# Kernel optimization log

Measured on AMD Instinct MI355X. Metric: run time of the kernel, lower is better.

Reference implementation:

```python
import jax, jax.numpy as jnp
import numpy as np

EMB = 1024
HEAD = 64
B = 4
S = 4096


def setup_inputs() -> dict:
    key = jax.random.key(0)
    ks = jax.random.split(key, 7)
    std = 1.0 / np.sqrt(EMB)
    return {
        "x": jax.random.normal(ks[0], (B, S, EMB), dtype=jnp.float32),
        "Wq": jax.random.uniform(ks[1], (EMB, HEAD), jnp.float32, -std, std),
        "bq": jax.random.uniform(ks[2], (HEAD,), jnp.float32, -std, std),
        "Wk": jax.random.uniform(ks[3], (EMB, HEAD), jnp.float32, -std, std),
        "bk": jax.random.uniform(ks[4], (HEAD,), jnp.float32, -std, std),
        "Wv": jax.random.uniform(ks[5], (EMB, HEAD), jnp.float32, -std, std),
        "bv": jax.random.uniform(ks[6], (HEAD,), jnp.float32, -std, std),
    }


def reference(x, Wq, bq, Wk, bk, Wv, bv):
    # Q, K, V: [B, S, HEAD]
    Q = x @ Wq + bq
    K = x @ Wk + bk
    V = x @ Wv + bv
    scale = 1.0 / jnp.sqrt(jnp.asarray(HEAD, dtype=Q.dtype))
    # scores: [B, S, S]
    scores = jnp.einsum("bqd,bkd->bqk", Q, K) * scale
    seq = x.shape[1]
    # original mask = tril(randn) sliced; masked_fill where mask==0 => causal
    causal = jnp.tril(jnp.ones((seq, seq), dtype=bool))
    scores = jnp.where(causal, scores, -jnp.inf)
    attn = jax.nn.softmax(scores, axis=-1)
    return jnp.einsum("bqk,bkd->bqd", attn, V)
```

## Files before the change

### kernel.cpp

```cpp
#include <hip/hip_runtime.h>
#include <stdint.h>

#define S_LEN 4096
#define EMB   1024
#define HEAD  64

typedef short bf16x8 __attribute__((ext_vector_type(8)));
typedef float f32x4  __attribute__((ext_vector_type(4)));
typedef float f32x16 __attribute__((ext_vector_type(16)));
typedef unsigned short ushort8 __attribute__((ext_vector_type(8)));

#define QSCALE 0.18033688011112042f

__device__ __forceinline__ unsigned short f2bf(float f) {
    union { float f; uint32_t u; } v; v.f = f;
    uint32_t r = v.u + 0x7fffu + ((v.u >> 16) & 1u);
    return (unsigned short)(r >> 16);
}

__device__ __forceinline__ int cvtpk_bf16(float lo, float hi_) {
    int r;
    asm("v_cvt_pk_bf16_f32 %0, %1, %2" : "=v"(r) : "v"(lo), "v"(hi_));
    return r;
}

__device__ __forceinline__ void gload_lds16(const void* g, void* l) {
    __builtin_amdgcn_global_load_lds(
        (const __attribute__((address_space(1))) void*)g,
        (__attribute__((address_space(3))) void*)l, 16, 0, 0);
}


__global__ void wprep_kernel(const float* __restrict__ Wq,
                             const float* __restrict__ Wk,
                             const float* __restrict__ Wv,
                             unsigned short* __restrict__ wt) {
    __shared__ float t[64][65];
    const int tid = threadIdx.x;
    const int m   = blockIdx.x >> 4;
    const int kcb = blockIdx.x & 15;
    const int k0  = kcb << 6;
    const float* W = (m == 0) ? Wq : (m == 1) ? Wk : Wv;
    for (int i = 0; i < 4; ++i) {
        const int k  = (tid >> 4) + i * 16;
        const int n4 = (tid & 15) << 2;
        float4 v = *(const float4*)&W[(k0 + k) * 64 + n4];
        t[k][n4 + 0] = v.x; t[k][n4 + 1] = v.y;
        t[k][n4 + 2] = v.z; t[k][n4 + 3] = v.w;
    }
    __syncthreads();
    const int n = tid >> 2, kq = (tid & 3) << 4;
    __align__(16) unsigned short u[16];
    for (int i = 0; i < 16; ++i) u[i] = f2bf(t[kq + i][n]);
    const int nimg = m * 64 + n;
    const int base = kcb * 12288 + nimg * 64;
    const int c0   = (kq >> 3) ^ (n & 7);
    const int c1   = ((kq >> 3) + 1) ^ (n & 7);
    *(int4*)&wt[base + c0 * 8] = *(int4*)&u[0];
    *(int4*)&wt[base + c1 * 8] = *(int4*)&u[8];
}

__global__ __launch_bounds__(512, 2) void qkv_kernel(
    const float* __restrict__ x, const unsigned short* __restrict__ wt,
    const float* __restrict__ bq, const float* __restrict__ bk,
    const float* __restrict__ bv,
    unsigned short* __restrict__ Qp, unsigned short* __restrict__ Kp,
    unsigned short* __restrict__ Vt) {

    __shared__ __align__(16) unsigned short xs[2][64 * 72];
    __shared__ __align__(16) unsigned short ws[2][12288];

    const int tid  = threadIdx.x;
    const int lane = tid & 63;
    const int w    = tid >> 6;
    const int wm   = w & 1;
    const int wn   = w >> 1;
    const int quad = lane >> 4;
    const int lid  = lane & 15;
    const int row0 = blockIdx.x * 64;

    f32x4 acc[2][3];
    for (int mf = 0; mf < 2; ++mf)
        for (int nf = 0; nf < 3; ++nf) acc[mf][nf] = (f32x4){0.f, 0.f, 0.f, 0.f};

#define STAGE(BUF, KC)                                                         \
    do {                                                                       \
        {             \
            int rr = tid >> 3, c8 = (tid & 7) << 3;                            \
            const float* xp = &x[(row0 + rr) * EMB + (KC) * 64 + c8];          \
            float4 v0 = *(const float4*)xp;                                    \
            float4 v1 = *(const float4*)(xp + 4);                              \
            ushort8 u;                                                         \
            u[0] = f2bf(v0.x); u[1] = f2bf(v0.y);                              \
            u[2] = f2bf(v0.z); u[3] = f2bf(v0.w);                              \
            u[4] = f2bf(v1.x); u[5] = f2bf(v1.y);                              \
            u[6] = f2bf(v1.z); u[7] = f2bf(v1.w);                              \
            *(ushort8*)&xs[BUF][rr * 72 + c8] = u;                             \
        }                                                                      \
        {          \
            const unsigned short* gs = &wt[(KC) * 12288 + w * 1536 + lane * 8];\
            gload_lds16(gs,        &ws[BUF][w * 1536]);                        \
            gload_lds16(gs +  512, &ws[BUF][w * 1536 +  512]);                 \
            gload_lds16(gs + 1024, &ws[BUF][w * 1536 + 1024]);                 \
        }                                                                      \
    } while (0)

    STAGE(0, 0);
    __syncthreads();

    for (int kc = 0; kc < 16; ++kc) {
        const int cur = kc & 1;
        if (kc + 1 < 16) STAGE(cur ^ 1, kc + 1);
        for (int kk = 0; kk < 2; ++kk) {
            bf16x8 a0 = *(const bf16x8*)&xs[cur][(wm * 32 + lid) * 72 + kk * 32 + quad * 8];
            bf16x8 a1 = *(const bf16x8*)&xs[cur][(wm * 32 + 16 + lid) * 72 + kk * 32 + quad * 8];
            const int swz = ((((kk << 2) | quad) ^ (lid & 7)) << 3);
            for (int nf = 0; nf < 3; ++nf) {
                const int n = wn * 48 + nf * 16 + lid;
                bf16x8 bfr = *(const bf16x8*)&ws[cur][n * 64 + swz];
                acc[0][nf] = __builtin_amdgcn_mfma_f32_16x16x32_bf16(a0, bfr, acc[0][nf], 0, 0, 0);
                acc[1][nf] = __builtin_amdgcn_mfma_f32_16x16x32_bf16(a1, bfr, acc[1][nf], 0, 0, 0);
            }
        }
        __syncthreads();
    }
#undef STAGE

    for (int mf = 0; mf < 2; ++mf)
        for (int nf = 0; nf < 3; ++nf) {
            const int col = wn * 48 + nf * 16 + lid;
            const int mid = col >> 6;
            const int lc  = col & 63;
            const float bias = (mid == 0) ? bq[lc] : (mid == 1) ? bk[lc] : bv[lc];
            const int rb = row0 + wm * 32 + mf * 16 + quad * 4;
            f32x4 v = acc[mf][nf];
            if (mid < 2) {
                const int base = ((rb >> 5) << 11) + ((lc >> 3) << 8)
                               + ((rb & 31) << 3) + (lc & 7);
                unsigned short* P = (mid == 0) ? Qp : Kp;
                const float sc = (mid == 0) ? QSCALE : 1.0f;
                for (int j = 0; j < 4; ++j)
                    P[base + j * 8] = f2bf((v[j] + bias) * sc);
            } else {
                const int bb = rb >> 12, s = rb & 4095;
                ushort4 u;
                u.x = f2bf(v[0] + bias); u.y = f2bf(v[1] + bias);
                u.z = f2bf(v[2] + bias); u.w = f2bf(v[3] + bias);
                *(ushort4*)&Vt[bb * 262144 + (s >> 3) * 512 + lc * 8 + (s & 7)] = u;
            }
        }
}

__global__ __launch_bounds__(1024, 1) void flash_kernel(
    const unsigned short* __restrict__ Qp, const unsigned short* __restrict__ Kp,
    const unsigned short* __restrict__ Vt, float* __restrict__ out) {

    __shared__ __align__(16) float Obuf[16][32][66];
    __shared__ float lbuf[16][32];

    const int tid  = threadIdx.x;
    const int lane = tid & 63;
    const int w    = tid >> 6;
    const int hi   = lane >> 5;
    const int l5   = lane & 31;

    const int l  = blockIdx.x;
    const int x  = l & 7;
    const int b  = x & 3;
    const int p  = ((x >> 2) << 5) + (l >> 3);

    const unsigned short* Kb = &Kp[b * 262144];
    const unsigned short* Vb = &Vt[b * 262144];

    for (int half = 0; half < 2; ++half) {
        const int qt = half ? p : 127 - p;
        const int q0 = qt * 32;
        const int nt = qt + 1;

        bf16x8 qf[4];
#pragma unroll
        for (int dk = 0; dk < 4; ++dk)
            qf[dk] = *(const bf16x8*)&Qp[((b << 7) + qt) * 2048
                                         + (dk * 2 + hi) * 256 + l5 * 8];

        f32x16 O0 = {}, O1 = {};
        float ls = 0.f;

        int t = w;
        bf16x8 kf[4];
        if (t < nt) {
#pragma unroll
            for (int dk = 0; dk < 4; ++dk)
                kf[dk] = *(const bf16x8*)&Kb[t * 2048 + (dk * 2 + hi) * 256 + l5 * 8];
        }

        while (t < nt) {
            const int kt = t << 5;
            bf16x8 vf[2][2];
#pragma unroll
            for (int kc = 0; kc < 2; ++kc)
#pragma unroll
                for (int dh = 0; dh < 2; ++dh)
                    vf[dh][kc] = *(const bf16x8*)&Vb[(t * 4 + kc * 2 + hi) * 512
                                                     + (dh * 32 + l5) * 8];

            __builtin_amdgcn_s_setprio(1);
            f32x16 st = {};
#pragma unroll
            for (int dk = 0; dk < 4; ++dk)
                st = __builtin_amdgcn_mfma_f32_32x32x16_bf16(kf[dk], qf[dk], st, 0, 0, 0);
            __builtin_amdgcn_s_setprio(0);

            const int tn = t + 16;
            if (tn < nt) {
#pragma unroll
                for (int dk = 0; dk < 4; ++dk)
                    kf[dk] = *(const bf16x8*)&Kb[tn * 2048 + (dk * 2 + hi) * 256 + l5 * 8];
            }

            if (t == nt - 1) {
#pragma unroll
                for (int rr = 0; rr < 16; ++rr) {
                    const int key = kt + (rr & 3) + 8 * (rr >> 2) + 4 * hi;
                    if (key > q0 + l5) st[rr] = -1e30f;
                }
            }

#pragma unroll
            for (int kc = 0; kc < 2; ++kc) {
                const int c8 = kc * 8;
                float ev[8];
#pragma unroll
                for (int i = 0; i < 8; ++i) ev[i] = __builtin_amdgcn_exp2f(st[c8 + i]);
                ls += ((ev[0] + ev[1]) + (ev[2] + ev[3])) +
                      ((ev[4] + ev[5]) + (ev[6] + ev[7]));
                const int p0 = cvtpk_bf16(ev[0], ev[1]);
                const int p1 = cvtpk_bf16(ev[2], ev[3]);
                const int p2 = cvtpk_bf16(ev[4], ev[5]);
                const int p3 = cvtpk_bf16(ev[6], ev[7]);
                auto s02 = __builtin_amdgcn_permlane32_swap(p0, p2, false, false);
                auto s13 = __builtin_amdgcn_permlane32_swap(p1, p3, false, false);
                union { int wd[4]; bf16x8 v; } pf;
                pf.wd[0] = s02[0]; pf.wd[1] = s13[0];
                pf.wd[2] = s02[1]; pf.wd[3] = s13[1];
                __builtin_amdgcn_s_setprio(1);
                O0 = __builtin_amdgcn_mfma_f32_32x32x16_bf16(pf.v, vf[0][kc], O0, 0, 0, 0);
                O1 = __builtin_amdgcn_mfma_f32_32x32x16_bf16(pf.v, vf[1][kc], O1, 0, 0, 0);
                __builtin_amdgcn_s_setprio(0);
            }
            t = tn;
        }

        const float lt = ls + __shfl_xor(ls, 32);
#pragma unroll
        for (int rr = 0; rr < 16; ++rr) {
            const int row = (rr & 3) + 8 * (rr >> 2) + 4 * hi;
            Obuf[w][row][l5]      = O0[rr];
            Obuf[w][row][32 + l5] = O1[rr];
        }
        if (lane < 32) lbuf[w][l5] = lt;
        __syncthreads();

        const int col = tid & 63;
        const int r0  = tid >> 6;
        for (int ii = 0; ii < 2; ++ii) {
            const int row = r0 + ii * 16;
            float o = 0.f, lsum = 0.f;
            for (int ww = 0; ww < 16; ++ww) {
                o    += Obuf[ww][row][col];
                lsum += lbuf[ww][row];
            }
            out[(b * S_LEN + q0 + row) * 64 + col] = o / lsum;
        }
        __syncthreads();
    }
}

extern "C" void kernel_launch(void* const* d_in, const int* in_sizes, int n_in,
                              void* d_out, int out_size, void* d_ws, size_t ws_size,
                              hipStream_t stream) {
    const float* x  = (const float*)d_in[0];
    const float* Wq = (const float*)d_in[1];
    const float* bq = (const float*)d_in[2];
    const float* Wk = (const float*)d_in[3];
    const float* bk = (const float*)d_in[4];
    const float* Wv = (const float*)d_in[5];
    const float* bv = (const float*)d_in[6];
    float* out = (float*)d_out;

    unsigned short* wt = (unsigned short*)d_ws;
    unsigned short* Qp = wt + 196608;
    unsigned short* Kp = Qp + 1048576;
    unsigned short* Vt = Kp + 1048576;

    hipLaunchKernelGGL(wprep_kernel, dim3(48), dim3(256), 0, stream, Wq, Wk, Wv, wt);
    hipLaunchKernelGGL(qkv_kernel, dim3(256), dim3(512), 0, stream,
                       x, wt, bq, bk, bv, Qp, Kp, Vt);
    hipLaunchKernelGGL(flash_kernel, dim3(256), dim3(1024), 0, stream,
                       Qp, Kp, Vt, out);
}
```

Before: 139.9 us.

## Halve flash block to 8 waves, each processing two key tiles per iteration

The flash kernel now uses 512 threads (8 waves) instead of 16. Each wave handles two interleaved key tiles per loop iteration, issuing both QK MFMA chains before the softmax/PV work to expose more instruction-level parallelism and prefetch two K tiles ahead. The cross-wave LDS reduction shrinks to 8 partials. This trades thread-level parallelism for per-wave ILP and raises register pressure, with fewer waves available to hide memory latency.

Result: faster. 135.8 us (-2.9%).

```diff
diff --git a/kernel.cpp b/kernel.cpp
--- a/kernel.cpp
+++ b/kernel.cpp
@@ -151,12 +151,64 @@
         }
 }
 
-__global__ __launch_bounds__(1024, 1) void flash_kernel(
+__device__ __forceinline__ void load_k(const unsigned short* Kb, int t,
+                                       int hi, int l5, bf16x8 (&kf)[4]) {
+#pragma unroll
+    for (int dk = 0; dk < 4; ++dk)
+        kf[dk] = *(const bf16x8*)&Kb[t * 2048 + (dk * 2 + hi) * 256 + l5 * 8];
+}
+
+__device__ __forceinline__ void load_v(const unsigned short* Vb, int t,
+                                       int hi, int l5, bf16x8 (&vf)[2][2]) {
+#pragma unroll
+    for (int kc = 0; kc < 2; ++kc)
+#pragma unroll
+        for (int dh = 0; dh < 2; ++dh)
+            vf[dh][kc] = *(const bf16x8*)&Vb[(t * 4 + kc * 2 + hi) * 512
+                                             + (dh * 32 + l5) * 8];
+}
+
+__device__ __forceinline__ void mask_diag(f32x16& st, int kt, int q0,
+                                          int hi, int l5) {
+#pragma unroll
+    for (int rr = 0; rr < 16; ++rr) {
+        const int key = kt + (rr & 3) + 8 * (rr >> 2) + 4 * hi;
+        if (key > q0 + l5) st[rr] = -1e30f;
+    }
+}
+
+__device__ __forceinline__ void softmax_pv(const f32x16& st, const bf16x8 (&vf)[2][2],
+                                           f32x16& O0, f32x16& O1, float& ls) {
+#pragma unroll
+    for (int kc = 0; kc < 2; ++kc) {
+        const int c8 = kc * 8;
+        float ev[8];
+#pragma unroll
+        for (int i = 0; i < 8; ++i) ev[i] = __builtin_amdgcn_exp2f(st[c8 + i]);
+        ls += ((ev[0] + ev[1]) + (ev[2] + ev[3])) +
+              ((ev[4] + ev[5]) + (ev[6] + ev[7]));
+        const int p0 = cvtpk_bf16(ev[0], ev[1]);
+        const int p1 = cvtpk_bf16(ev[2], ev[3]);
+        const int p2 = cvtpk_bf16(ev[4], ev[5]);
+        const int p3 = cvtpk_bf16(ev[6], ev[7]);
+        auto s02 = __builtin_amdgcn_permlane32_swap(p0, p2, false, false);
+        auto s13 = __builtin_amdgcn_permlane32_swap(p1, p3, false, false);
+        union { int wd[4]; bf16x8 v; } pf;
+        pf.wd[0] = s02[0]; pf.wd[1] = s13[0];
+        pf.wd[2] = s02[1]; pf.wd[3] = s13[1];
+        __builtin_amdgcn_s_setprio(1);
+        O0 = __builtin_amdgcn_mfma_f32_32x32x16_bf16(pf.v, vf[0][kc], O0, 0, 0, 0);
+        O1 = __builtin_amdgcn_mfma_f32_32x32x16_bf16(pf.v, vf[1][kc], O1, 0, 0, 0);
+        __builtin_amdgcn_s_setprio(0);
+    }
+}
+
+__global__ __launch_bounds__(512, 1) void flash_kernel(
     const unsigned short* __restrict__ Qp, const unsigned short* __restrict__ Kp,
     const unsigned short* __restrict__ Vt, float* __restrict__ out) {
 
-    __shared__ __align__(16) float Obuf[16][32][66];
-    __shared__ float lbuf[16][32];
+    __shared__ __align__(16) float Obuf[8][32][66];
+    __shared__ float lbuf[8][32];
 
     const int tid  = threadIdx.x;
     const int lane = tid & 63;
@@ -187,68 +239,44 @@
         float ls = 0.f;
 
         int t = w;
-        bf16x8 kf[4];
-        if (t < nt) {
+        bf16x8 kf1[4], kf2[4];
+        if (t < nt)     load_k(Kb, t,     hi, l5, kf1);
+        if (t + 8 < nt) load_k(Kb, t + 8, hi, l5, kf2);
+
+        while (t < nt) {
+            const int t2   = t + 8;
+            const bool has2 = (t2 < nt);
+
+            bf16x8 vf1[2][2];
+            load_v(Vb, t, hi, l5, vf1);
+            __builtin_amdgcn_s_setprio(1);
+            f32x16 st1 = {};
 #pragma unroll
             for (int dk = 0; dk < 4; ++dk)
-                kf[dk] = *(const bf16x8*)&Kb[t * 2048 + (dk * 2 + hi) * 256 + l5 * 8];
-        }
-
-        while (t < nt) {
-            const int kt = t << 5;
-            bf16x8 vf[2][2];
-#pragma unroll
-            for (int kc = 0; kc < 2; ++kc)
-#pragma unroll
-                for (int dh = 0; dh < 2; ++dh)
-                    vf[dh][kc] = *(const bf16x8*)&Vb[(t * 4 + kc * 2 + hi) * 512
-                                                     + (dh * 32 + l5) * 8];
-
-            __builtin_amdgcn_s_setprio(1);
-            f32x16 st = {};
-#pragma unroll
-            for (int dk = 0; dk < 4; ++dk)
-                st = __builtin_amdgcn_mfma_f32_32x32x16_bf16(kf[dk], qf[dk], st, 0, 0, 0);
+                st1 = __builtin_amdgcn_mfma_f32_32x32x16_bf16(kf1[dk], qf[dk], st1, 0, 0, 0);
             __builtin_amdgcn_s_setprio(0);
 
-            const int tn = t + 16;
-            if (tn < nt) {
+            bf16x8 vf2[2][2];
+            f32x16 st2 = {};
+            if (has2) {
+                load_v(Vb, t2, hi, l5, vf2);
+                __builtin_amdgcn_s_setprio(1);
 #pragma unroll
                 for (int dk = 0; dk < 4; ++dk)
-                    kf[dk] = *(const bf16x8*)&Kb[tn * 2048 + (dk * 2 + hi) * 256 + l5 * 8];
-            }
-
-            if (t == nt - 1) {
-#pragma unroll
-                for (int rr = 0; rr < 16; ++rr) {
-                    const int key = kt + (rr & 3) + 8 * (rr >> 2) + 4 * hi;
-                    if (key > q0 + l5) st[rr] = -1e30f;
-                }
-            }
-
-#pragma unroll
-            for (int kc = 0; kc < 2; ++kc) {
-                const int c8 = kc * 8;
-                float ev[8];
-#pragma unroll
-                for (int i = 0; i < 8; ++i) ev[i] = __builtin_amdgcn_exp2f(st[c8 + i]);
-                ls += ((ev[0] + ev[1]) + (ev[2] + ev[3])) +
-                      ((ev[4] + ev[5]) + (ev[6] + ev[7]));
-                const int p0 = cvtpk_bf16(ev[0], ev[1]);
-                const int p1 = cvtpk_bf16(ev[2], ev[3]);
-                const int p2 = cvtpk_bf16(ev[4], ev[5]);
-                const int p3 = cvtpk_bf16(ev[6], ev[7]);
-                auto s02 = __builtin_amdgcn_permlane32_swap(p0, p2, false, false);
-                auto s13 = __builtin_amdgcn_permlane32_swap(p1, p3, false, false);
-                union { int wd[4]; bf16x8 v; } pf;
-                pf.wd[0] = s02[0]; pf.wd[1] = s13[0];
-                pf.wd[2] = s02[1]; pf.wd[3] = s13[1];
-                __builtin_amdgcn_s_setprio(1);
-                O0 = __builtin_amdgcn_mfma_f32_32x32x16_bf16(pf.v, vf[0][kc], O0, 0, 0, 0);
-                O1 = __builtin_amdgcn_mfma_f32_32x32x16_bf16(pf.v, vf[1][kc], O1, 0, 0, 0);
+                    st2 = __builtin_amdgcn_mfma_f32_32x32x16_bf16(kf2[dk], qf[dk], st2, 0, 0, 0);
                 __builtin_amdgcn_s_setprio(0);
             }
-            t = tn;
+
+            if (t + 16 < nt) load_k(Kb, t + 16, hi, l5, kf1);
+            if (t + 24 < nt) load_k(Kb, t + 24, hi, l5, kf2);
+
+            if (t == nt - 1) mask_diag(st1, t << 5, q0, hi, l5);
+            softmax_pv(st1, vf1, O0, O1, ls);
+            if (has2) {
+                if (t2 == nt - 1) mask_diag(st2, t2 << 5, q0, hi, l5);
+                softmax_pv(st2, vf2, O0, O1, ls);
+            }
+            t += 16;
         }
 
         const float lt = ls + __shfl_xor(ls, 32);
@@ -263,10 +291,10 @@
 
         const int col = tid & 63;
         const int r0  = tid >> 6;
-        for (int ii = 0; ii < 2; ++ii) {
-            const int row = r0 + ii * 16;
+        for (int ii = 0; ii < 4; ++ii) {
+            const int row = r0 + ii * 8;
             float o = 0.f, lsum = 0.f;
-            for (int ww = 0; ww < 16; ++ww) {
+            for (int ww = 0; ww < 8; ++ww) {
                 o    += Obuf[ww][row][col];
                 lsum += lbuf[ww][row];
             }
@@ -296,6 +324,6 @@
     hipLaunchKernelGGL(wprep_kernel, dim3(48), dim3(256), 0, stream, Wq, Wk, Wv, wt);
     hipLaunchKernelGGL(qkv_kernel, dim3(256), dim3(512), 0, stream,
                        x, wt, bq, bk, bv, Qp, Kp, Vt);
-    hipLaunchKernelGGL(flash_kernel, dim3(256), dim3(1024), 0, stream,
+    hipLaunchKernelGGL(flash_kernel, dim3(256), dim3(512), 0, stream,
                        Qp, Kp, Vt, out);
 }
```
